# Performance work log

Measured on AMD Instinct MI355X. Metric: run time of the kernel, lower is better.

The kernel has to match this reference:

```python
import jax, jax.numpy as jnp
import numpy as np

N, E, D_IN, D_H, D_OUT, W = 100000, 1600000, 128, 128, 128, 3
HTC_W, TEMP = 0.01, 1.0  # curvature c = 1.0


def _project(x):
    n = jnp.maximum(jnp.linalg.norm(x, axis=-1, keepdims=True), 1e-12)
    return x * jnp.minimum((1.0 - 1e-5) / n, 1.0)


def _artanh(x):
    x = jnp.clip(x, -1.0 + 1e-6, 1.0 - 1e-6)
    return 0.5 * (jnp.log1p(x) - jnp.log1p(-x))


def _expmap0(v):
    n = jnp.maximum(jnp.linalg.norm(v, axis=-1, keepdims=True), 1e-12)
    return _project(jnp.tanh(n) * v / n)


def _logmap0(y):
    y = _project(y)
    n = jnp.maximum(jnp.linalg.norm(y, axis=-1, keepdims=True), 1e-12)
    return _artanh(n) * y / n


def setup_inputs() -> dict:
    key = jax.random.key(0)
    ks = jax.random.split(key, 24)
    x = jax.random.normal(ks[0], (N, D_IN), dtype=jnp.float32)
    edge_index = jax.random.randint(ks[1], (2, E), 0, N)
    t = jax.random.uniform(ks[2], (E,), dtype=jnp.float32)
    prev_hyp = _project(jax.random.normal(ks[3], (N, D_OUT), dtype=jnp.float32) * 0.05)
    lengths = jax.random.randint(ks[4], (N,), 0, W + 1)
    valid_mask = jnp.arange(W)[None, :] < lengths[:, None]  # front-filled deque
    hist_hyp = _project(jax.random.normal(ks[5], (N, W, D_OUT), dtype=jnp.float32) * 0.05)
    hist_hyp = hist_hyp * valid_mask[..., None].astype(jnp.float32)  # padded slots are zero

    def lin(k, dout, din):
        return jax.random.normal(k, (dout, din), dtype=jnp.float32) / np.sqrt(din)

    params = dict(
        w_time=jax.random.normal(ks[6], (D_IN,), dtype=jnp.float32),
        b_time=jnp.zeros((D_IN,), jnp.float32),
        W0_l=lin(ks[7], D_H, D_IN), b0_l=jnp.zeros((D_H,), jnp.float32), W0_r=lin(ks[8], D_H, D_IN),
        W1_l=lin(ks[9], D_OUT, D_H), b1_l=jnp.zeros((D_OUT,), jnp.float32), W1_r=lin(ks[10], D_OUT, D_H),
        W_ih=lin(ks[11], 3 * D_OUT, D_OUT), W_hh=lin(ks[12], 3 * D_OUT, D_OUT),
        b_ih=jnp.zeros((3 * D_OUT,), jnp.float32), b_hh=jnp.zeros((3 * D_OUT,), jnp.float32),
        Wq=lin(ks[13], D_OUT, D_OUT), Wk=lin(ks[14], D_OUT, D_OUT), Wv=lin(ks[15], D_OUT, D_OUT),
    )
    return dict(x=x, edge_index=edge_index, t=t, prev_hyp=prev_hyp,
                hist_hyp=hist_hyp, valid_mask=valid_mask, **params)


def reference(x, edge_index, t, prev_hyp, hist_hyp, valid_mask,
              w_time, b_time, W0_l, b0_l, W0_r, W1_l, b1_l, W1_r,
              W_ih, W_hh, b_ih, b_hh, Wq, Wk, Wv):
    n = x.shape[0]
    src, dst = edge_index[0], edge_index[1]
    ones_e = jnp.ones_like(t)
    # per-node mean event time over incident edges (src and dst both count)
    nt = jax.ops.segment_sum(t, src, n) + jax.ops.segment_sum(t, dst, n)
    cnt = jax.ops.segment_sum(ones_e, src, n) + jax.ops.segment_sum(ones_e, dst, n)
    node_time = nt / jnp.maximum(cnt, 1.0)
    x = x + jnp.cos(node_time[:, None] * w_time[None, :] + b_time[None, :])
    # SAGEConv (mean aggr over incoming edges): out = W_l @ mean_j x_j + b + W_r @ x_i
    deg = jnp.maximum(jax.ops.segment_sum(ones_e, dst, n), 1.0)[:, None]
    agg0 = jax.ops.segment_sum(x[src], dst, n) / deg
    h = jax.nn.relu(agg0 @ W0_l.T + b0_l + x @ W0_r.T)
    agg1 = jax.ops.segment_sum(h[src], dst, n) / deg
    h_now = agg1 @ W1_l.T + b1_l + h @ W1_r.T  # tangent-space current embedding

    prev_tan = _logmap0(prev_hyp)
    # ragged history attention (padded + masked)
    hist_tan = _logmap0(hist_hyp)                       # [N, W, D]
    q = h_now @ Wq.T                                    # [N, D]
    k = hist_tan @ Wk.T                                 # [N, W, D]
    v = hist_tan @ Wv.T
    score = jnp.einsum('nwd,nd->nw', k, q) / (np.sqrt(D_OUT) * max(TEMP, 1e-6))
    has_hist = valid_mask.any(axis=-1, keepdims=True)
    score = jnp.where(valid_mask, score, -jnp.inf)
    score = jnp.where(has_hist, score, 0.0)
    alpha = jax.nn.softmax(score, axis=-1)
    alpha = jnp.where(has_hist, alpha, 0.0)
    ctx = jnp.einsum('nw,nwd->nd', alpha, v)

    # GRUCell(input=h_now, hidden=prev_tan + ctx)
    hidden = prev_tan + ctx
    gi = h_now @ W_ih.T + b_ih
    gh = hidden @ W_hh.T + b_hh
    i_r, i_z, i_n = jnp.split(gi, 3, axis=-1)
    h_r, h_z, h_n = jnp.split(gh, 3, axis=-1)
    r = jax.nn.sigmoid(i_r + h_r)
    z = jax.nn.sigmoid(i_z + h_z)
    nn_ = jnp.tanh(i_n + r * h_n)
    h_tan = (1.0 - z) * nn_ + z * hidden
    h_hyp = _expmap0(h_tan)

    # hyperbolic temporal consistency aux loss (c = 1)
    x_sq = jnp.sum(h_hyp * h_hyp, axis=-1)
    y_sq = jnp.sum(prev_hyp * prev_hyp, axis=-1)
    diff_sq = jnp.sum((h_hyp - prev_hyp) ** 2, axis=-1)
    denom = jnp.maximum((1.0 - x_sq) * (1.0 - y_sq), 1e-8)
    zarg = jnp.maximum(1.0 + 2.0 * diff_sq / denom, 1.0 + 1e-6)
    dist = jnp.arccosh(zarg)
    valid_prev = (jnp.sum(jnp.abs(prev_hyp), axis=-1) > 0).astype(dist.dtype)
    aux = HTC_W * jnp.sum(dist * valid_prev) / jnp.maximum(jnp.sum(valid_prev), 1.0)
    aux = jnp.where(jnp.any(valid_prev > 0), aux, 0.0)
    return h_hyp, aux
```

## Files before the change

kernel.cpp:

```cpp
#include <hip/hip_runtime.h>
#include <math.h>


typedef _Float16 f16x8 __attribute__((ext_vector_type(8)));
typedef _Float16 f16x4 __attribute__((ext_vector_type(4)));
typedef _Float16 f16x2 __attribute__((ext_vector_type(2)));
typedef float f32x4 __attribute__((ext_vector_type(4)));

__device__ __forceinline__ float wsum(float v) {
#pragma unroll
  for (int off = 1; off < 64; off <<= 1) v += __shfl_xor(v, off, 64);
  return v;
}

__device__ __forceinline__ void fsplit(float x, _Float16& h, _Float16& l) {
  h = (_Float16)x;
  l = (_Float16)(x - (float)h);
}

__device__ __forceinline__ float logmap_scale(float nrm2) {
  float n0 = fmaxf(sqrtf(nrm2), 1e-12f);
  float sp = fminf((1.0f - 1e-5f) / n0, 1.0f);
  float np = fmaxf(n0 * sp, 1e-12f);
  float a  = fminf(np, 1.0f - 1e-6f);
  float at = 0.5f * (log1pf(a) - log1pf(-a));
  return sp * at / np;
}

__global__ void k_edge(const int* __restrict__ ei, const float* __restrict__ t,
                       unsigned long long* __restrict__ packed, int E) {
  int e = blockIdx.x * 256 + threadIdx.x;
  if (e >= E) return;
  int s = ei[e], d = ei[E + e];
  unsigned long long tf =
      (unsigned long long)__float2uint_rn(t[e] * 16777216.0f);
  unsigned long long encs = tf | (1ULL << 40);
  atomicAdd(&packed[s], encs);
  atomicAdd(&packed[d], encs | (1ULL << 52));
}

__global__ void k_scan1(const unsigned long long* __restrict__ packed,
                        int* __restrict__ rowptr, int* __restrict__ bsum, int N) {
  __shared__ int s[256];
  int t = threadIdx.x;
  int base = blockIdx.x * 1024 + t * 4;
  int v[4]; int loc = 0;
#pragma unroll
  for (int j = 0; j < 4; ++j) {
    int i = base + j;
    v[j] = (i < N) ? (int)(packed[i] >> 52) : 0;
    loc += v[j];
  }
  s[t] = loc; __syncthreads();
  for (int off = 1; off < 256; off <<= 1) {
    int x = (t >= off) ? s[t - off] : 0; __syncthreads();
    s[t] += x; __syncthreads();
  }
  int run = s[t] - loc;
#pragma unroll
  for (int j = 0; j < 4; ++j) { int i = base + j; if (i < N) rowptr[i] = run; run += v[j]; }
  if (t == 255) bsum[blockIdx.x] = s[255];
}

__global__ void k_scan2(const int* __restrict__ bsum, int* __restrict__ boff, int nb) {
  __shared__ int s[128];
  int t = threadIdx.x;
  int v = (t < nb) ? bsum[t] : 0;
  s[t] = v; __syncthreads();
  for (int off = 1; off < 128; off <<= 1) {
    int x = (t >= off) ? s[t - off] : 0; __syncthreads();
    s[t] += x; __syncthreads();
  }
  boff[t] = s[t] - v;
}

__global__ void k_scan3(int* __restrict__ rowptr, const int* __restrict__ boff, int N, int E) {
  int i = blockIdx.x * 256 + threadIdx.x;
  if (i < N) rowptr[i] += boff[i >> 10];
  if (i == 0) rowptr[N] = E;
}

__global__ void k_scatter(const int* __restrict__ ei, const int* __restrict__ rowptr,
                          int* __restrict__ cursor, int* __restrict__ eidx, int E) {
  int e = blockIdx.x * 256 + threadIdx.x;
  if (e >= E) return;
  int s = ei[e], d = ei[E + e];
  int p = rowptr[d] + atomicAdd(&cursor[d], 1);
  eidx[p] = s;
}

__global__ void k_time(const float* __restrict__ x,
                       const unsigned long long* __restrict__ packed,
                       const float* __restrict__ wt,
                       const float* __restrict__ bt,
                       _Float16* __restrict__ outH, _Float16* __restrict__ outL, int N) {
  int id = blockIdx.x * 256 + threadIdx.x;
  if (id >= N * 32) return;
  int n = id >> 5, q = id & 31;
  unsigned long long p = packed[n];
  float tsum = (float)(p & 0xFFFFFFFFFFULL) * 5.9604644775390625e-8f;
  int c = (int)((p >> 40) & 0xFFF);
  float tm = tsum / fmaxf((float)c, 1.0f);
  float4 xv = ((const float4*)x)[id];
  float4 wv = ((const float4*)wt)[q];
  float4 bv = ((const float4*)bt)[q];
  float o[4];
  o[0] = xv.x + cosf(tm * wv.x + bv.x);
  o[1] = xv.y + cosf(tm * wv.y + bv.y);
  o[2] = xv.z + cosf(tm * wv.z + bv.z);
  o[3] = xv.w + cosf(tm * wv.w + bv.w);
  f16x4 vh, vl;
#pragma unroll
  for (int j = 0; j < 4; ++j) { _Float16 h, l; fsplit(o[j], h, l); vh[j] = h; vl[j] = l; }
  *(f16x4*)&outH[(size_t)id * 4] = vh;
  *(f16x4*)&outL[(size_t)id * 4] = vl;
}

__global__ void k_agg(const _Float16* __restrict__ XH, const _Float16* __restrict__ XL,
                      const int* __restrict__ rowptr,
                      const int* __restrict__ eidx, _Float16* __restrict__ outH,
                      _Float16* __restrict__ outL, int N) {
  int wid = threadIdx.x >> 6, lane = threadIdx.x & 63;
  int n = blockIdx.x * 4 + wid;
  if (n >= N) return;
  int s0 = rowptr[n], s1 = rowptr[n + 1];
  size_t lo2 = (size_t)lane * 2;
  float ax0 = 0.f, ay0 = 0.f, ax1 = 0.f, ay1 = 0.f;
  float ax2 = 0.f, ay2 = 0.f, ax3 = 0.f, ay3 = 0.f;
  int e = s0;
  for (; e + 4 <= s1; e += 4) {
    int i0 = eidx[e], i1 = eidx[e + 1], i2 = eidx[e + 2], i3 = eidx[e + 3];
    f16x2 h0 = *(const f16x2*)&XH[(size_t)i0 * 128 + lo2];
    f16x2 l0 = *(const f16x2*)&XL[(size_t)i0 * 128 + lo2];
    f16x2 h1 = *(const f16x2*)&XH[(size_t)i1 * 128 + lo2];
    f16x2 l1 = *(const f16x2*)&XL[(size_t)i1 * 128 + lo2];
    f16x2 h2 = *(const f16x2*)&XH[(size_t)i2 * 128 + lo2];
    f16x2 l2 = *(const f16x2*)&XL[(size_t)i2 * 128 + lo2];
    f16x2 h3 = *(const f16x2*)&XH[(size_t)i3 * 128 + lo2];
    f16x2 l3 = *(const f16x2*)&XL[(size_t)i3 * 128 + lo2];
    ax0 += (float)h0[0] + (float)l0[0]; ay0 += (float)h0[1] + (float)l0[1];
    ax1 += (float)h1[0] + (float)l1[0]; ay1 += (float)h1[1] + (float)l1[1];
    ax2 += (float)h2[0] + (float)l2[0]; ay2 += (float)h2[1] + (float)l2[1];
    ax3 += (float)h3[0] + (float)l3[0]; ay3 += (float)h3[1] + (float)l3[1];
  }
  float ax = (ax0 + ax1) + (ax2 + ax3);
  float ay = (ay0 + ay1) + (ay2 + ay3);
  for (; e < s1; ++e) {
    int s = eidx[e];
    f16x2 vh = *(const f16x2*)&XH[(size_t)s * 128 + lo2];
    f16x2 vl = *(const f16x2*)&XL[(size_t)s * 128 + lo2];
    ax += (float)vh[0] + (float)vl[0];
    ay += (float)vh[1] + (float)vl[1];
  }
  float sc = 1.0f / fmaxf((float)(s1 - s0), 1.0f);
  _Float16 hx, lx, hy, ly;
  fsplit(ax * sc, hx, lx); fsplit(ay * sc, hy, ly);
  f16x2 vh = {hx, hy}, vl = {lx, ly};
  *(f16x2*)&outH[(size_t)n * 128 + lo2] = vh;
  *(f16x2*)&outL[(size_t)n * 128 + lo2] = vl;
}

__global__ void k_prep(const float* __restrict__ W0l, const float* __restrict__ W0r,
                       const float* __restrict__ W1l, const float* __restrict__ W1r,
                       const float* __restrict__ Wv,  const float* __restrict__ Wih,
                       const float* __restrict__ Whh, const float* __restrict__ bih,
                       const float* __restrict__ bhh,
                       _Float16* __restrict__ W0H, _Float16* __restrict__ W0L,
                       _Float16* __restrict__ W1H, _Float16* __restrict__ W1L,
                       _Float16* __restrict__ WvH, _Float16* __restrict__ WvL,
                       _Float16* __restrict__ WzH, _Float16* __restrict__ WzL,
                       float* __restrict__ bz) {
  int id = blockIdx.x * 256 + threadIdx.x;
  if (id < 32768) {
    int c = id >> 8, k = id & 255;
    float v0 = (k < 128) ? W0l[c * 128 + k] : W0r[c * 128 + (k - 128)];
    float v1 = (k < 128) ? W1l[c * 128 + k] : W1r[c * 128 + (k - 128)];
    fsplit(v0, W0H[id], W0L[id]);
    fsplit(v1, W1H[id], W1L[id]);
  }
  if (id < 16384) {
    fsplit(Wv[id], WvH[id], WvL[id]);
  }
  if (id < 131072) {
    int c = id >> 8, k = id & 255;
    float v;
    if (c < 256)      v = (k < 128) ? Wih[c * 128 + k] : Whh[c * 128 + (k - 128)];
    else if (c < 384) v = (k < 128) ? Wih[c * 128 + k] : 0.f;
    else              v = (k < 128) ? 0.f : Whh[(c - 128) * 128 + (k - 128)];
    fsplit(v, WzH[id], WzL[id]);
  }
  if (id < 512) {
    float v;
    if (id < 256)      v = bih[id] + bhh[id];
    else if (id < 384) v = bih[id];
    else               v = bhh[id - 128];
    bz[id] = v;
  }
}

__global__ void k_ct(const float* __restrict__ Wk, const float* __restrict__ Wq,
                     _Float16* __restrict__ CtH, _Float16* __restrict__ CtL) {
  int id = blockIdx.x * 256 + threadIdx.x;
  if (id >= 16384) return;
  int c = id >> 7, k = id & 127;
  float s = 0.f;
  for (int j = 0; j < 128; ++j) s += Wk[j * 128 + c] * Wq[j * 128 + k];
  fsplit(s, CtH[id], CtL[id]);
}

__global__ void k_lognorm(const float* __restrict__ Y, float* __restrict__ scale, int N) {
  int wid = threadIdx.x >> 6, lane = threadIdx.x & 63;
  int n = blockIdx.x * 4 + wid;
  if (n >= N) return;
  float2 y = ((const float2*)Y)[(size_t)n * 64 + lane];
  float nrm2 = wsum(y.x * y.x + y.y * y.y);
  if (lane == 0) scale[n] = logmap_scale(nrm2);
}

__global__ __launch_bounds__(256)
void k_mm(const _Float16* __restrict__ A1H, const _Float16* __restrict__ A1L,
          const _Float16* __restrict__ A2H, const _Float16* __restrict__ A2L,
          const _Float16* __restrict__ WH,  const _Float16* __restrict__ WL,
          const float* __restrict__ bias,   const float* __restrict__ addb,
          const float* __restrict__ scalev,
          float* __restrict__ outF, _Float16* __restrict__ outH,
          _Float16* __restrict__ outL,
          int Nrows, int Ktot, int Ctot, int relu) {
  __shared__ _Float16 sA[2][128][64];
  __shared__ _Float16 sW[2][128][64];
  const int tid = threadIdx.x;
  const int lane = tid & 63;
  const int wv = tid >> 6;
  const int wr = wv >> 1, wc = wv & 1;
  const int laneR = lane & 15, laneG = lane >> 4;
  const int n0 = blockIdx.x * 128;
  const int c0 = blockIdx.y * 128;

  f32x4 acc[4][4];
#pragma unroll
  for (int mi = 0; mi < 4; ++mi)
#pragma unroll
    for (int ni = 0; ni < 4; ++ni)
#pragma unroll
      for (int j = 0; j < 4; ++j) acc[mi][ni][j] = 0.f;

  const int nslab = Ktot >> 6;
  for (int s = 0; s < nslab; ++s) {
    int kglob = s << 6;
    const _Float16* aH = (kglob < 128) ? A1H : A2H;
    const _Float16* aL = (kglob < 128) ? A1L : A2L;
    int kc = kglob & 127;
    __syncthreads();
#pragma unroll
    for (int it = 0; it < 4; ++it) {
      int idx = tid + (it << 8);
      int r = idx >> 3, chunk = idx & 7;
      int cs = (chunk ^ (r & 7)) << 3;
      int kq = chunk << 3;
      int n = n0 + r;
      f16x8 vh, vl;
      if (n < Nrows) {
        vh = *(const f16x8*)&aH[(size_t)n * 128 + kc + kq];
        vl = *(const f16x8*)&aL[(size_t)n * 128 + kc + kq];
      } else {
#pragma unroll
        for (int j = 0; j < 8; ++j) { vh[j] = (_Float16)0; vl[j] = (_Float16)0; }
      }
      *(f16x8*)&sA[0][r][cs] = vh;
      *(f16x8*)&sA[1][r][cs] = vl;
      int c = c0 + r;
      f16x8 wh = *(const f16x8*)&WH[(size_t)c * Ktot + kglob + kq];
      f16x8 wl = *(const f16x8*)&WL[(size_t)c * Ktot + kglob + kq];
      *(f16x8*)&sW[0][r][cs] = wh;
      *(f16x8*)&sW[1][r][cs] = wl;
    }
    __syncthreads();
#pragma unroll
    for (int kk = 0; kk < 2; ++kk) {
      f16x8 ah[4], al[4], bh[4], bl[4];
      int kch = (kk << 2) + laneG;
#pragma unroll
      for (int m = 0; m < 4; ++m) {
        int row = wr * 64 + m * 16 + laneR;
        int ko = (kch ^ (row & 7)) << 3;
        ah[m] = *(const f16x8*)&sA[0][row][ko];
        al[m] = *(const f16x8*)&sA[1][row][ko];
      }
#pragma unroll
      for (int n = 0; n < 4; ++n) {
        int row = wc * 64 + n * 16 + laneR;
        int ko = (kch ^ (row & 7)) << 3;
        bh[n] = *(const f16x8*)&sW[0][row][ko];
        bl[n] = *(const f16x8*)&sW[1][row][ko];
      }
#pragma unroll
      for (int m = 0; m < 4; ++m)
#pragma unroll
        for (int n = 0; n < 4; ++n) {
          acc[m][n] = __builtin_amdgcn_mfma_f32_16x16x32_f16(ah[m], bh[n], acc[m][n], 0, 0, 0);
          acc[m][n] = __builtin_amdgcn_mfma_f32_16x16x32_f16(al[m], bh[n], acc[m][n], 0, 0, 0);
          acc[m][n] = __builtin_amdgcn_mfma_f32_16x16x32_f16(ah[m], bl[n], acc[m][n], 0, 0, 0);
        }
    }
  }
#pragma unroll
  for (int m = 0; m < 4; ++m) {
#pragma unroll
    for (int n = 0; n < 4; ++n) {
      int rbase = n0 + wr * 64 + m * 16 + laneG * 4;
      int c = c0 + wc * 64 + n * 16 + laneR;
      float bval = bias ? bias[c] : 0.f;
#pragma unroll
      for (int j = 0; j < 4; ++j) {
        int r = rbase + j;
        if (r >= Nrows) continue;
        float v = acc[m][n][j] + bval;
        if (addb) {
          float ab = addb[(size_t)r * Ctot + c];
          v += scalev ? ab * scalev[r] : ab;
        }
        if (relu) v = fmaxf(v, 0.f);
        if (outF) outF[(size_t)r * Ctot + c] = v;
        if (outH) {
          _Float16 h, l; fsplit(v, h, l);
          outH[(size_t)r * Ctot + c] = h;
          outL[(size_t)r * Ctot + c] = l;
        }
      }
    }
  }
}

__global__ __launch_bounds__(256, 2)
void k_uattn(const _Float16* __restrict__ AH, const _Float16* __restrict__ AL,
             const _Float16* __restrict__ WH, const _Float16* __restrict__ WL,
             const float* __restrict__ hist,
             _Float16* __restrict__ outH, _Float16* __restrict__ outL, int N) {
  __shared__ __align__(16) char smem[65536];
  _Float16 (*sA)[128][64] = (_Float16(*)[128][64])smem;
  _Float16 (*sW)[128][64] = (_Float16(*)[128][64])(smem + 32768);
  float (*uS)[128] = (float(*)[128])smem;
  const int tid = threadIdx.x;
  const int lane = tid & 63;
  const int wv = tid >> 6;
  const int wr = wv >> 1, wc = wv & 1;
  const int laneR = lane & 15, laneG = lane >> 4;
  const int n0 = blockIdx.x * 128;

  f32x4 acc[4][4];
#pragma unroll
  for (int mi = 0; mi < 4; ++mi)
#pragma unroll
    for (int ni = 0; ni < 4; ++ni)
#pragma unroll
      for (int j = 0; j < 4; ++j) acc[mi][ni][j] = 0.f;

  for (int s = 0; s < 2; ++s) {
    int kglob = s << 6;
    __syncthreads();
#pragma unroll
    for (int it = 0; it < 4; ++it) {
      int idx = tid + (it << 8);
      int r = idx >> 3, chunk = idx & 7;
      int cs = (chunk ^ (r & 7)) << 3;
      int kq = chunk << 3;
      int n = n0 + r;
      f16x8 vh, vl;
      if (n < N) {
        vh = *(const f16x8*)&AH[(size_t)n * 128 + kglob + kq];
        vl = *(const f16x8*)&AL[(size_t)n * 128 + kglob + kq];
      } else {
#pragma unroll
        for (int j = 0; j < 8; ++j) { vh[j] = (_Float16)0; vl[j] = (_Float16)0; }
      }
      *(f16x8*)&sA[0][r][cs] = vh;
      *(f16x8*)&sA[1][r][cs] = vl;
      f16x8 wh = *(const f16x8*)&WH[(size_t)r * 128 + kglob + kq];
      f16x8 wl = *(const f16x8*)&WL[(size_t)r * 128 + kglob + kq];
      *(f16x8*)&sW[0][r][cs] = wh;
      *(f16x8*)&sW[1][r][cs] = wl;
    }
    __syncthreads();
#pragma unroll
    for (int kk = 0; kk < 2; ++kk) {
      f16x8 ah[4], al[4], bh[4], bl[4];
      int kch = (kk << 2) + laneG;
#pragma unroll
      for (int m = 0; m < 4; ++m) {
        int row = wr * 64 + m * 16 + laneR;
        int ko = (kch ^ (row & 7)) << 3;
        ah[m] = *(const f16x8*)&sA[0][row][ko];
        al[m] = *(const f16x8*)&sA[1][row][ko];
      }
#pragma unroll
      for (int n = 0; n < 4; ++n) {
        int row = wc * 64 + n * 16 + laneR;
        int ko = (kch ^ (row & 7)) << 3;
        bh[n] = *(const f16x8*)&sW[0][row][ko];
        bl[n] = *(const f16x8*)&sW[1][row][ko];
      }
#pragma unroll
      for (int m = 0; m < 4; ++m)
#pragma unroll
        for (int n = 0; n < 4; ++n) {
          acc[m][n] = __builtin_amdgcn_mfma_f32_16x16x32_f16(ah[m], bh[n], acc[m][n], 0, 0, 0);
          acc[m][n] = __builtin_amdgcn_mfma_f32_16x16x32_f16(al[m], bh[n], acc[m][n], 0, 0, 0);
          acc[m][n] = __builtin_amdgcn_mfma_f32_16x16x32_f16(ah[m], bl[n], acc[m][n], 0, 0, 0);
        }
    }
  }
  __syncthreads();
#pragma unroll
  for (int m = 0; m < 4; ++m)
#pragma unroll
    for (int n = 0; n < 4; ++n) {
      int rl = wr * 64 + m * 16 + laneG * 4;
      int c = wc * 64 + n * 16 + laneR;
#pragma unroll
      for (int j = 0; j < 4; ++j) uS[rl + j][c] = acc[m][n][j];
    }
  __syncthreads();

  for (int i = 0; i < 32; ++i) {
    int rl = wv * 32 + i;
    int n = n0 + rl;
    if (n >= N) break;
    float2 u = *(const float2*)&uS[rl][lane * 2];
    float htx[3], hty[3], sc[3];
    bool val[3];
#pragma unroll
    for (int w = 0; w < 3; ++w) {
      float2 h = ((const float2*)hist)[((size_t)n * 3 + w) * 64 + lane];
      float nrm2 = wsum(h.x * h.x + h.y * h.y);
      val[w] = nrm2 > 0.f;
      float s = logmap_scale(nrm2);
      htx[w] = h.x * s; hty[w] = h.y * s;
      float d = wsum(htx[w] * u.x + hty[w] * u.y);
      sc[w] = d * 0.0883883476483184f;
    }
    float cx = 0.f, cy = 0.f;
    if (val[0] || val[1] || val[2]) {
      float m = -INFINITY;
#pragma unroll
      for (int w = 0; w < 3; ++w) if (val[w]) m = fmaxf(m, sc[w]);
      float a[3]; float ssum = 0.f;
#pragma unroll
      for (int w = 0; w < 3; ++w) { a[w] = val[w] ? expf(sc[w] - m) : 0.f; ssum += a[w]; }
      float inv = 1.f / ssum;
#pragma unroll
      for (int w = 0; w < 3; ++w) { cx += htx[w] * (a[w] * inv); cy += hty[w] * (a[w] * inv); }
    }
    _Float16 hx, lx, hy, ly;
    fsplit(cx, hx, lx); fsplit(cy, hy, ly);
    f16x2 vh = {hx, hy}, vl = {lx, ly};
    *(f16x2*)&outH[(size_t)n * 128 + lane * 2] = vh;
    *(f16x2*)&outL[(size_t)n * 128 + lane * 2] = vl;
  }
}

__global__ __launch_bounds__(256, 2)
void k_gru(const _Float16* __restrict__ P0H, const _Float16* __restrict__ P0L,
           const _Float16* __restrict__ P2H, const _Float16* __restrict__ P2L,
           const _Float16* __restrict__ WzH, const _Float16* __restrict__ WzL,
           const float* __restrict__ bz, const float* __restrict__ prev,
           float* __restrict__ out, float* __restrict__ pd,
           float* __restrict__ pv, int N) {
  __shared__ _Float16 sA[2][64][64];
  __shared__ _Float16 sW[2][128][64];
  __shared__ float rn1[64][2];
  __shared__ float rn3[64][2][3];
  __shared__ float distrow[64], validrow[64];
  const int tid = threadIdx.x;
  const int lane = tid & 63;
  const int wv = tid >> 6;
  const int wr = wv >> 1, wc = wv & 1;
  const int laneR = lane & 15, laneG = lane >> 4;
  const int n0 = blockIdx.x * 64;

  f32x4 acc[4][2][4];
#pragma unroll
  for (int q = 0; q < 4; ++q)
#pragma unroll
    for (int m = 0; m < 2; ++m)
#pragma unroll
      for (int n = 0; n < 4; ++n)
#pragma unroll
        for (int j = 0; j < 4; ++j) acc[q][m][n][j] = 0.f;

#define STAGE_W(Q)                                                          \
  {                                                                         \
    _Pragma("unroll")                                                       \
    for (int it = 0; it < 4; ++it) {                                        \
      int idx = tid + (it << 8);                                            \
      int r = idx >> 3, chunk = idx & 7;                                    \
      int cs = (chunk ^ (r & 7)) << 3;                                      \
      int kq = chunk << 3;                                                  \
      size_t wrow = (size_t)((Q)*128 + r);                                  \
      *(f16x8*)&sW[0][r][cs] = *(const f16x8*)&WzH[wrow * 256 + kglob + kq];\
      *(f16x8*)&sW[1][r][cs] = *(const f16x8*)&WzL[wrow * 256 + kglob + kq];\
    }                                                                       \
  }

#define COMPUTE_Q(Q)                                                        \
  {                                                                         \
    _Pragma("unroll")                                                       \
    for (int kk = 0; kk < 2; ++kk) {                                        \
      int kch = (kk << 2) + laneG;                                          \
      f16x8 ah[2], al[2], bh[4], bl[4];                                     \
      _Pragma("unroll")                                                     \
      for (int m = 0; m < 2; ++m) {                                         \
        int row = wr * 32 + m * 16 + laneR;                                 \
        int ko = (kch ^ (row & 7)) << 3;                                    \
        ah[m] = *(const f16x8*)&sA[0][row][ko];                             \
        al[m] = *(const f16x8*)&sA[1][row][ko];                             \
      }                                                                     \
      _Pragma("unroll")                                                     \
      for (int n = 0; n < 4; ++n) {                                         \
        int row = wc * 64 + n * 16 + laneR;                                 \
        int ko = (kch ^ (row & 7)) << 3;                                    \
        bh[n] = *(const f16x8*)&sW[0][row][ko];                             \
        bl[n] = *(const f16x8*)&sW[1][row][ko];                             \
      }                                                                     \
      _Pragma("unroll")                                                     \
      for (int m = 0; m < 2; ++m)                                           \
        _Pragma("unroll")                                                   \
        for (int n = 0; n < 4; ++n) {                                       \
          acc[Q][m][n] = __builtin_amdgcn_mfma_f32_16x16x32_f16(ah[m], bh[n], acc[Q][m][n], 0, 0, 0); \
          acc[Q][m][n] = __builtin_amdgcn_mfma_f32_16x16x32_f16(al[m], bh[n], acc[Q][m][n], 0, 0, 0); \
          acc[Q][m][n] = __builtin_amdgcn_mfma_f32_16x16x32_f16(ah[m], bl[n], acc[Q][m][n], 0, 0, 0); \
        }                                                                   \
    }                                                                       \
  }

#pragma unroll
  for (int s = 0; s < 4; ++s) {
    int kglob = s << 6;
    const _Float16* aH = (s < 2) ? P0H : P2H;
    const _Float16* aL = (s < 2) ? P0L : P2L;
    int kc = kglob & 127;
    __syncthreads();
#pragma unroll
    for (int it = 0; it < 2; ++it) {
      int idx = tid + (it << 8);
      int r = idx >> 3, chunk = idx & 7;
      int cs = (chunk ^ (r & 7)) << 3;
      int kq = chunk << 3;
      int n = n0 + r;
      f16x8 vh, vl;
      if (n < N) {
        vh = *(const f16x8*)&aH[(size_t)n * 128 + kc + kq];
        vl = *(const f16x8*)&aL[(size_t)n * 128 + kc + kq];
      } else {
#pragma unroll
        for (int j = 0; j < 8; ++j) { vh[j] = (_Float16)0; vl[j] = (_Float16)0; }
      }
      *(f16x8*)&sA[0][r][cs] = vh;
      *(f16x8*)&sA[1][r][cs] = vl;
    }
    STAGE_W(0);
    __syncthreads();
    COMPUTE_Q(0);
    __syncthreads();
    STAGE_W(1);
    __syncthreads();
    COMPUTE_Q(1);
    __syncthreads();
    if (s < 2) {
      STAGE_W(2);
      __syncthreads();
      COMPUTE_Q(2);
    } else {
      STAGE_W(3);
      __syncthreads();
      COMPUTE_Q(3);
    }
  }
#undef STAGE_W
#undef COMPUTE_Q

  float bz0[4], bz1[4], bz2[4], bz3[4];
#pragma unroll
  for (int n = 0; n < 4; ++n) {
    int d = wc * 64 + n * 16 + laneR;
    bz0[n] = bz[d]; bz1[n] = bz[128 + d]; bz2[n] = bz[256 + d]; bz3[n] = bz[384 + d];
  }
  float tv[2][4][4];
#pragma unroll
  for (int m = 0; m < 2; ++m)
#pragma unroll
    for (int n = 0; n < 4; ++n)
#pragma unroll
      for (int j = 0; j < 4; ++j) {
        int row = n0 + wr * 32 + m * 16 + laneG * 4 + j;
        int d = wc * 64 + n * 16 + laneR;
        float hid = 0.f;
        if (row < N) {
          size_t o = (size_t)row * 128 + d;
          hid = (float)P2H[o] + (float)P2L[o];
        }
        float gr = acc[0][m][n][j] + bz0[n];
        float gz = acc[1][m][n][j] + bz1[n];
        float gi = acc[2][m][n][j] + bz2[n];
        float gh = acc[3][m][n][j] + bz3[n];
        float rr = 1.f / (1.f + expf(-gr));
        float zz = 1.f / (1.f + expf(-gz));
        float nn = tanhf(gi + rr * gh);
        tv[m][n][j] = (1.f - zz) * nn + zz * hid;
      }
#pragma unroll
  for (int m = 0; m < 2; ++m)
#pragma unroll
    for (int j = 0; j < 4; ++j) {
      float p = 0.f;
#pragma unroll
      for (int n = 0; n < 4; ++n) p += tv[m][n][j] * tv[m][n][j];
#pragma unroll
      for (int off = 1; off < 16; off <<= 1) p += __shfl_xor(p, off, 64);
      if (laneR == 0) rn1[wr * 32 + m * 16 + laneG * 4 + j][wc] = p;
    }
  __syncthreads();
  float hv[2][4][4];
#pragma unroll
  for (int m = 0; m < 2; ++m)
#pragma unroll
    for (int j = 0; j < 4; ++j) {
      int rl = wr * 32 + m * 16 + laneG * 4 + j;
      int row = n0 + rl;
      float nv2 = rn1[rl][0] + rn1[rl][1];
      float nv = fmaxf(sqrtf(nv2), 1e-12f);
      float tn = tanhf(nv);
      float s1 = tn / nv;
      float nw = fmaxf(tn, 1e-12f);
      float sp = fminf((1.f - 1e-5f) / nw, 1.f);
      float scl = s1 * sp;
#pragma unroll
      for (int n = 0; n < 4; ++n) {
        float h = tv[m][n][j] * scl;
        hv[m][n][j] = h;
        int d = wc * 64 + n * 16 + laneR;
        if (row < N) out[(size_t)row * 128 + d] = h;
      }
    }
#pragma unroll
  for (int m = 0; m < 2; ++m)
#pragma unroll
    for (int j = 0; j < 4; ++j) {
      int rl = wr * 32 + m * 16 + laneG * 4 + j;
      int row = n0 + rl;
      float ys = 0.f, ds = 0.f, pa = 0.f;
#pragma unroll
      for (int n = 0; n < 4; ++n) {
        int d = wc * 64 + n * 16 + laneR;
        float p = (row < N) ? prev[(size_t)row * 128 + d] : 0.f;
        float h = hv[m][n][j];
        ys += p * p; ds += (h - p) * (h - p); pa += fabsf(p);
      }
#pragma unroll
      for (int off = 1; off < 16; off <<= 1) {
        ys += __shfl_xor(ys, off, 64);
        ds += __shfl_xor(ds, off, 64);
        pa += __shfl_xor(pa, off, 64);
      }
      if (laneR == 0) { rn3[rl][wc][0] = ys; rn3[rl][wc][1] = ds; rn3[rl][wc][2] = pa; }
    }
  __syncthreads();
  if (wc == 0 && laneR == 0) {
#pragma unroll
    for (int m = 0; m < 2; ++m)
#pragma unroll
      for (int j = 0; j < 4; ++j) {
        int rl = wr * 32 + m * 16 + laneG * 4 + j;
        int row = n0 + rl;
        float nv2 = rn1[rl][0] + rn1[rl][1];
        float nv = fmaxf(sqrtf(nv2), 1e-12f);
        float tn = tanhf(nv);
        float s1 = tn / nv;
        float nw = fmaxf(tn, 1e-12f);
        float sp = fminf((1.f - 1e-5f) / nw, 1.f);
        float scl = s1 * sp;
        float x_sq = scl * scl * nv2;
        float y_sq = rn3[rl][0][0] + rn3[rl][1][0];
        float d_sq = rn3[rl][0][1] + rn3[rl][1][1];
        float pab  = rn3[rl][0][2] + rn3[rl][1][2];
        float denom = fmaxf((1.f - x_sq) * (1.f - y_sq), 1e-8f);
        float zarg = fmaxf(1.f + 2.f * d_sq / denom, 1.f + 1e-6f);
        float dist = acoshf(zarg);
        float valid = (pab > 0.f && row < N) ? 1.f : 0.f;
        distrow[rl] = dist * valid;
        validrow[rl] = valid;
      }
  }
  __syncthreads();
  if (tid < 64) {
    float dv = distrow[tid], vvv = validrow[tid];
    dv = wsum(dv); vvv = wsum(vvv);
    if (tid == 0) { pd[blockIdx.x] = dv; pv[blockIdx.x] = vvv; }
  }
}

__global__ void k_reduce(const float* __restrict__ pd, const float* __restrict__ pv,
                         float* __restrict__ aux_out, int nparts) {
  __shared__ float sd[256], sv[256];
  float a = 0.f, b = 0.f;
  for (int i = threadIdx.x; i < nparts; i += 256) { a += pd[i]; b += pv[i]; }
  sd[threadIdx.x] = a; sv[threadIdx.x] = b; __syncthreads();
  for (int off = 128; off > 0; off >>= 1) {
    if (threadIdx.x < off) { sd[threadIdx.x] += sd[threadIdx.x + off]; sv[threadIdx.x] += sv[threadIdx.x + off]; }
    __syncthreads();
  }
  if (threadIdx.x == 0) {
    float aux = (sv[0] > 0.f) ? 0.01f * sd[0] / fmaxf(sv[0], 1.f) : 0.f;
    aux_out[0] = aux;
  }
}

extern "C" void kernel_launch(void* const* d_in, const int* in_sizes, int n_in,
                              void* d_out, int out_size, void* d_ws, size_t ws_size,
                              hipStream_t stream) {
  const float* x      = (const float*)d_in[0];
  const int*   ei     = (const int*)  d_in[1];
  const float* t      = (const float*)d_in[2];
  const float* prev   = (const float*)d_in[3];
  const float* hist   = (const float*)d_in[4];
  const float* w_time = (const float*)d_in[6];
  const float* b_time = (const float*)d_in[7];
  const float* W0l    = (const float*)d_in[8];
  const float* b0l    = (const float*)d_in[9];
  const float* W0r    = (const float*)d_in[10];
  const float* W1l    = (const float*)d_in[11];
  const float* b1l    = (const float*)d_in[12];
  const float* W1r    = (const float*)d_in[13];
  const float* Wih    = (const float*)d_in[14];
  const float* Whh    = (const float*)d_in[15];
  const float* bih    = (const float*)d_in[16];
  const float* bhh    = (const float*)d_in[17];
  const float* Wq     = (const float*)d_in[18];
  const float* Wk     = (const float*)d_in[19];
  const float* Wv     = (const float*)d_in[20];

  const int N = in_sizes[0] / 128;
  const int E = in_sizes[1] / 2;
  const int NB4 = (N + 3) / 4;
  const int NB1 = (N + 1023) / 1024;
  const int NBG = (N + 63) / 64;

  char* wbase = (char*)d_ws;
  size_t off = 0;
  auto alloc = [&](size_t bytes) -> void* {
    off = (off + 255) & ~(size_t)255;
    void* p = wbase + off; off += bytes; return p;
  };
  unsigned long long* packed = (unsigned long long*)alloc((size_t)N * 8);
  int*   cursor = (int*)  alloc((size_t)N * 4);
  size_t zero_bytes = off;
  int*   rowptr = (int*)  alloc((size_t)(N + 1) * 4);
  int*   bsum   = (int*)  alloc(512);
  int*   boff   = (int*)  alloc(512);
  int*   eidx   = (int*)  alloc((size_t)E * 4);
  _Float16* W0H = (_Float16*)alloc(32768 * 2);
  _Float16* W0L = (_Float16*)alloc(32768 * 2);
  _Float16* W1H = (_Float16*)alloc(32768 * 2);
  _Float16* W1L = (_Float16*)alloc(32768 * 2);
  _Float16* CtH = (_Float16*)alloc(16384 * 2);
  _Float16* CtL = (_Float16*)alloc(16384 * 2);
  _Float16* WvH = (_Float16*)alloc(16384 * 2);
  _Float16* WvL = (_Float16*)alloc(16384 * 2);
  _Float16* WzH = (_Float16*)alloc(131072 * 2);
  _Float16* WzL = (_Float16*)alloc(131072 * 2);
  float* bz     = (float*)alloc(512 * 4);
  float* scale  = (float*)alloc((size_t)N * 4);
  _Float16* P0H = (_Float16*)alloc((size_t)N * 128 * 2);
  _Float16* P0L = (_Float16*)alloc((size_t)N * 128 * 2);
  _Float16* P1H = (_Float16*)alloc((size_t)N * 128 * 2);
  _Float16* P1L = (_Float16*)alloc((size_t)N * 128 * 2);
  _Float16* P2H = (_Float16*)alloc((size_t)N * 128 * 2);
  _Float16* P2L = (_Float16*)alloc((size_t)N * 128 * 2);
  float* pd = (float*)alloc((size_t)NBG * 4);
  float* pv = (float*)alloc((size_t)NBG * 4);
  (void)ws_size; (void)n_in; (void)out_size;

  float* out_h   = (float*)d_out;
  float* out_aux = out_h + (size_t)N * 128;

  hipMemsetAsync(d_ws, 0, zero_bytes, stream);

  k_prep<<<512, 256, 0, stream>>>(W0l, W0r, W1l, W1r, Wv, Wih, Whh, bih, bhh,
                                  W0H, W0L, W1H, W1L, WvH, WvL, WzH, WzL, bz);
  k_ct<<<64, 256, 0, stream>>>(Wk, Wq, CtH, CtL);
  k_lognorm<<<NB4, 256, 0, stream>>>(prev, scale, N);

  int ebl = (E + 255) / 256;
  k_edge<<<ebl, 256, 0, stream>>>(ei, t, packed, E);
  k_scan1<<<NB1, 256, 0, stream>>>(packed, rowptr, bsum, N);
  k_scan2<<<1, 128, 0, stream>>>(bsum, boff, NB1);
  k_scan3<<<(N + 255) / 256, 256, 0, stream>>>(rowptr, boff, N, E);
  k_scatter<<<ebl, 256, 0, stream>>>(ei, rowptr, cursor, eidx, E);

  k_time<<<(N * 32 + 255) / 256, 256, 0, stream>>>(x, packed, w_time, b_time,
                                                   P0H, P0L, N);
  k_agg<<<NB4, 256, 0, stream>>>(P0H, P0L, rowptr, eidx, P1H, P1L, N);
  dim3 gb((N + 127) / 128, 1);
  k_mm<<<gb, 256, 0, stream>>>(P1H, P1L, P0H, P0L, W0H, W0L, b0l, nullptr, nullptr,
                               nullptr, P2H, P2L, N, 256, 128, 1);
  k_agg<<<NB4, 256, 0, stream>>>(P2H, P2L, rowptr, eidx, P1H, P1L, N);
  k_mm<<<gb, 256, 0, stream>>>(P1H, P1L, P2H, P2L, W1H, W1L, b1l, nullptr, nullptr,
                               nullptr, P0H, P0L, N, 256, 128, 0);
  k_uattn<<<gb, 256, 0, stream>>>(P0H, P0L, CtH, CtL, hist, P1H, P1L, N);
  k_mm<<<gb, 256, 0, stream>>>(P1H, P1L, nullptr, nullptr, WvH, WvL, nullptr, prev,
                               scale, nullptr, P2H, P2L, N, 128, 128, 0);
  k_gru<<<NBG, 256, 0, stream>>>(P0H, P0L, P2H, P2L, WzH, WzL, bz, prev,
                                 out_h, pd, pv, N);
  k_reduce<<<1, 256, 0, stream>>>(pd, pv, out_aux, NBG);
}
```

Before: 1.215 ms.

## Interleave hi/lo f16 splits per row and fuse layer-1 GEMM with query projection

The separate hi and lo f16 buffers become one interleaved row of 256 halves per node. The gather in k_agg then fetches hi and lo together in one 8-byte load per lane, touching one contiguous 512-byte row instead of two separate rows. The layer-1 GEMM is fused with the Ct projection in a new k_mmu kernel that writes the split output and an fp32 U buffer. The attention softmax becomes its own per-node kernel, k_attn. This trades an extra fp32 N×128 buffer write and read, plus another launch, for fewer scattered gather transactions and less work packed into one kernel.

```diff
diff --git a/kernel.cpp b/kernel.cpp
--- a/kernel.cpp
+++ b/kernel.cpp
@@ -93,7 +93,7 @@
                        const unsigned long long* __restrict__ packed,
                        const float* __restrict__ wt,
                        const float* __restrict__ bt,
-                       _Float16* __restrict__ outH, _Float16* __restrict__ outL, int N) {
+                       _Float16* __restrict__ out, int N) {
   int id = blockIdx.x * 256 + threadIdx.x;
   if (id >= N * 32) return;
   int n = id >> 5, q = id & 31;
@@ -112,52 +112,56 @@
   f16x4 vh, vl;
 #pragma unroll
   for (int j = 0; j < 4; ++j) { _Float16 h, l; fsplit(o[j], h, l); vh[j] = h; vl[j] = l; }
-  *(f16x4*)&outH[(size_t)id * 4] = vh;
-  *(f16x4*)&outL[(size_t)id * 4] = vl;
-}
-
-__global__ void k_agg(const _Float16* __restrict__ XH, const _Float16* __restrict__ XL,
-                      const int* __restrict__ rowptr,
-                      const int* __restrict__ eidx, _Float16* __restrict__ outH,
-                      _Float16* __restrict__ outL, int N) {
+  *(f16x4*)&out[(size_t)n * 256 + q * 4] = vh;
+  *(f16x4*)&out[(size_t)n * 256 + 128 + q * 4] = vl;
+}
+
+__global__ void k_agg(const _Float16* __restrict__ X, const int* __restrict__ rowptr,
+                      const int* __restrict__ eidx, _Float16* __restrict__ out, int N) {
   int wid = threadIdx.x >> 6, lane = threadIdx.x & 63;
   int n = blockIdx.x * 4 + wid;
   if (n >= N) return;
   int s0 = rowptr[n], s1 = rowptr[n + 1];
-  size_t lo2 = (size_t)lane * 2;
-  float ax0 = 0.f, ay0 = 0.f, ax1 = 0.f, ay1 = 0.f;
-  float ax2 = 0.f, ay2 = 0.f, ax3 = 0.f, ay3 = 0.f;
+  size_t lo4 = (size_t)lane * 4;
+  float a0[4] = {0, 0, 0, 0}, a1[4] = {0, 0, 0, 0};
+  float a2[4] = {0, 0, 0, 0}, a3[4] = {0, 0, 0, 0};
   int e = s0;
   for (; e + 4 <= s1; e += 4) {
     int i0 = eidx[e], i1 = eidx[e + 1], i2 = eidx[e + 2], i3 = eidx[e + 3];
-    f16x2 h0 = *(const f16x2*)&XH[(size_t)i0 * 128 + lo2];
-    f16x2 l0 = *(const f16x2*)&XL[(size_t)i0 * 128 + lo2];
-    f16x2 h1 = *(const f16x2*)&XH[(size_t)i1 * 128 + lo2];
-    f16x2 l1 = *(const f16x2*)&XL[(size_t)i1 * 128 + lo2];
-    f16x2 h2 = *(const f16x2*)&XH[(size_t)i2 * 128 + lo2];
-    f16x2 l2 = *(const f16x2*)&XL[(size_t)i2 * 128 + lo2];
-    f16x2 h3 = *(const f16x2*)&XH[(size_t)i3 * 128 + lo2];
-    f16x2 l3 = *(const f16x2*)&XL[(size_t)i3 * 128 + lo2];
-    ax0 += (float)h0[0] + (float)l0[0]; ay0 += (float)h0[1] + (float)l0[1];
-    ax1 += (float)h1[0] + (float)l1[0]; ay1 += (float)h1[1] + (float)l1[1];
-    ax2 += (float)h2[0] + (float)l2[0]; ay2 += (float)h2[1] + (float)l2[1];
-    ax3 += (float)h3[0] + (float)l3[0]; ay3 += (float)h3[1] + (float)l3[1];
-  }
-  float ax = (ax0 + ax1) + (ax2 + ax3);
-  float ay = (ay0 + ay1) + (ay2 + ay3);
+    f16x4 v0 = *(const f16x4*)&X[(size_t)i0 * 256 + lo4];
+    f16x4 v1 = *(const f16x4*)&X[(size_t)i1 * 256 + lo4];
+    f16x4 v2 = *(const f16x4*)&X[(size_t)i2 * 256 + lo4];
+    f16x4 v3 = *(const f16x4*)&X[(size_t)i3 * 256 + lo4];
+#pragma unroll
+    for (int j = 0; j < 4; ++j) {
+      a0[j] += (float)v0[j]; a1[j] += (float)v1[j];
+      a2[j] += (float)v2[j]; a3[j] += (float)v3[j];
+    }
+  }
+  float a[4];
+#pragma unroll
+  for (int j = 0; j < 4; ++j) a[j] = (a0[j] + a1[j]) + (a2[j] + a3[j]);
   for (; e < s1; ++e) {
     int s = eidx[e];
-    f16x2 vh = *(const f16x2*)&XH[(size_t)s * 128 + lo2];
-    f16x2 vl = *(const f16x2*)&XL[(size_t)s * 128 + lo2];
-    ax += (float)vh[0] + (float)vl[0];
-    ay += (float)vh[1] + (float)vl[1];
-  }
-  float sc = 1.0f / fmaxf((float)(s1 - s0), 1.0f);
-  _Float16 hx, lx, hy, ly;
-  fsplit(ax * sc, hx, lx); fsplit(ay * sc, hy, ly);
-  f16x2 vh = {hx, hy}, vl = {lx, ly};
-  *(f16x2*)&outH[(size_t)n * 128 + lo2] = vh;
-  *(f16x2*)&outL[(size_t)n * 128 + lo2] = vl;
+    f16x4 v = *(const f16x4*)&X[(size_t)s * 256 + lo4];
+#pragma unroll
+    for (int j = 0; j < 4; ++j) a[j] += (float)v[j];
+  }
+  float lov[4];
+#pragma unroll
+  for (int j = 0; j < 4; ++j) lov[j] = __shfl(a[j], lane + 32, 64);
+  if (lane < 32) {
+    float sc = 1.0f / fmaxf((float)(s1 - s0), 1.0f);
+    f16x4 vh, vl;
+#pragma unroll
+    for (int j = 0; j < 4; ++j) {
+      float v = (a[j] + lov[j]) * sc;
+      _Float16 h, l; fsplit(v, h, l);
+      vh[j] = h; vl[j] = l;
+    }
+    *(f16x4*)&out[(size_t)n * 256 + lane * 4] = vh;
+    *(f16x4*)&out[(size_t)n * 256 + 128 + lane * 4] = vl;
+  }
 }
 
 __global__ void k_prep(const float* __restrict__ W0l, const float* __restrict__ W0r,
@@ -218,13 +222,11 @@
 }
 
 __global__ __launch_bounds__(256)
-void k_mm(const _Float16* __restrict__ A1H, const _Float16* __restrict__ A1L,
-          const _Float16* __restrict__ A2H, const _Float16* __restrict__ A2L,
+void k_mm(const _Float16* __restrict__ A1, const _Float16* __restrict__ A2,
           const _Float16* __restrict__ WH,  const _Float16* __restrict__ WL,
           const float* __restrict__ bias,   const float* __restrict__ addb,
           const float* __restrict__ scalev,
-          float* __restrict__ outF, _Float16* __restrict__ outH,
-          _Float16* __restrict__ outL,
+          float* __restrict__ outF, _Float16* __restrict__ outS,
           int Nrows, int Ktot, int Ctot, int relu) {
   __shared__ _Float16 sA[2][128][64];
   __shared__ _Float16 sW[2][128][64];
@@ -247,8 +249,7 @@
   const int nslab = Ktot >> 6;
   for (int s = 0; s < nslab; ++s) {
     int kglob = s << 6;
-    const _Float16* aH = (kglob < 128) ? A1H : A2H;
-    const _Float16* aL = (kglob < 128) ? A1L : A2L;
+    const _Float16* Ax = (kglob < 128) ? A1 : A2;
     int kc = kglob & 127;
     __syncthreads();
 #pragma unroll
@@ -260,8 +261,8 @@
       int n = n0 + r;
       f16x8 vh, vl;
       if (n < Nrows) {
-        vh = *(const f16x8*)&aH[(size_t)n * 128 + kc + kq];
-        vl = *(const f16x8*)&aL[(size_t)n * 128 + kc + kq];
+        vh = *(const f16x8*)&Ax[(size_t)n * 256 + kc + kq];
+        vl = *(const f16x8*)&Ax[(size_t)n * 256 + 128 + kc + kq];
       } else {
 #pragma unroll
         for (int j = 0; j < 8; ++j) { vh[j] = (_Float16)0; vl[j] = (_Float16)0; }
@@ -321,25 +322,24 @@
         }
         if (relu) v = fmaxf(v, 0.f);
         if (outF) outF[(size_t)r * Ctot + c] = v;
-        if (outH) {
+        if (outS) {
           _Float16 h, l; fsplit(v, h, l);
-          outH[(size_t)r * Ctot + c] = h;
-          outL[(size_t)r * Ctot + c] = l;
+          outS[(size_t)r * 256 + c] = h;
+          outS[(size_t)r * 256 + 128 + c] = l;
         }
       }
     }
   }
 }
 
-__global__ __launch_bounds__(256, 2)
-void k_uattn(const _Float16* __restrict__ AH, const _Float16* __restrict__ AL,
-             const _Float16* __restrict__ WH, const _Float16* __restrict__ WL,
-             const float* __restrict__ hist,
-             _Float16* __restrict__ outH, _Float16* __restrict__ outL, int N) {
-  __shared__ __align__(16) char smem[65536];
-  _Float16 (*sA)[128][64] = (_Float16(*)[128][64])smem;
-  _Float16 (*sW)[128][64] = (_Float16(*)[128][64])(smem + 32768);
-  float (*uS)[128] = (float(*)[128])smem;
+__global__ __launch_bounds__(256)
+void k_mmu(const _Float16* __restrict__ A1, const _Float16* __restrict__ A2,
+           const _Float16* __restrict__ WH, const _Float16* __restrict__ WL,
+           const _Float16* __restrict__ CtH, const _Float16* __restrict__ CtL,
+           const float* __restrict__ bias,
+           _Float16* __restrict__ outS, float* __restrict__ outU, int Nrows) {
+  __shared__ _Float16 sA[2][128][64];
+  __shared__ _Float16 sW[2][128][64];
   const int tid = threadIdx.x;
   const int lane = tid & 63;
   const int wv = tid >> 6;
@@ -355,8 +355,10 @@
 #pragma unroll
       for (int j = 0; j < 4; ++j) acc[mi][ni][j] = 0.f;
 
-  for (int s = 0; s < 2; ++s) {
+  for (int s = 0; s < 4; ++s) {
     int kglob = s << 6;
+    const _Float16* Ax = (kglob < 128) ? A1 : A2;
+    int kc = kglob & 127;
     __syncthreads();
 #pragma unroll
     for (int it = 0; it < 4; ++it) {
@@ -366,17 +368,17 @@
       int kq = chunk << 3;
       int n = n0 + r;
       f16x8 vh, vl;
-      if (n < N) {
-        vh = *(const f16x8*)&AH[(size_t)n * 128 + kglob + kq];
-        vl = *(const f16x8*)&AL[(size_t)n * 128 + kglob + kq];
+      if (n < Nrows) {
+        vh = *(const f16x8*)&Ax[(size_t)n * 256 + kc + kq];
+        vl = *(const f16x8*)&Ax[(size_t)n * 256 + 128 + kc + kq];
       } else {
 #pragma unroll
         for (int j = 0; j < 8; ++j) { vh[j] = (_Float16)0; vl[j] = (_Float16)0; }
       }
       *(f16x8*)&sA[0][r][cs] = vh;
       *(f16x8*)&sA[1][r][cs] = vl;
-      f16x8 wh = *(const f16x8*)&WH[(size_t)r * 128 + kglob + kq];
-      f16x8 wl = *(const f16x8*)&WL[(size_t)r * 128 + kglob + kq];
+      f16x8 wh = *(const f16x8*)&WH[(size_t)r * 256 + kglob + kq];
+      f16x8 wl = *(const f16x8*)&WL[(size_t)r * 256 + kglob + kq];
       *(f16x8*)&sW[0][r][cs] = wh;
       *(f16x8*)&sW[1][r][cs] = wl;
     }
@@ -409,58 +411,134 @@
         }
     }
   }
-  __syncthreads();
-#pragma unroll
-  for (int m = 0; m < 4; ++m)
+
+  f32x4 accU[4][4];
+#pragma unroll
+  for (int mi = 0; mi < 4; ++mi)
+#pragma unroll
+    for (int ni = 0; ni < 4; ++ni)
+#pragma unroll
+      for (int j = 0; j < 4; ++j) accU[mi][ni][j] = 0.f;
+
+  for (int us = 0; us < 2; ++us) {
+    __syncthreads();
+    if (wc == us) {
+#pragma unroll
+      for (int m = 0; m < 4; ++m)
+#pragma unroll
+        for (int n = 0; n < 4; ++n) {
+          int kp = n * 16 + laneR;
+          float bval = bias[us * 64 + n * 16 + laneR];
+#pragma unroll
+          for (int j = 0; j < 4; ++j) {
+            int row = wr * 64 + m * 16 + laneG * 4 + j;
+            float v = acc[m][n][j] + bval;
+            _Float16 h, l; fsplit(v, h, l);
+            int cs = ((kp >> 3) ^ (row & 7)) * 8 + (kp & 7);
+            sA[0][row][cs] = h;
+            sA[1][row][cs] = l;
+          }
+        }
+    }
+#pragma unroll
+    for (int it = 0; it < 4; ++it) {
+      int idx = tid + (it << 8);
+      int r = idx >> 3, chunk = idx & 7;
+      int cs = (chunk ^ (r & 7)) << 3;
+      int kq = chunk << 3;
+      *(f16x8*)&sW[0][r][cs] = *(const f16x8*)&CtH[(size_t)r * 128 + us * 64 + kq];
+      *(f16x8*)&sW[1][r][cs] = *(const f16x8*)&CtL[(size_t)r * 128 + us * 64 + kq];
+    }
+    __syncthreads();
+#pragma unroll
+    for (int kk = 0; kk < 2; ++kk) {
+      f16x8 ah[4], al[4], bh[4], bl[4];
+      int kch = (kk << 2) + laneG;
+#pragma unroll
+      for (int m = 0; m < 4; ++m) {
+        int row = wr * 64 + m * 16 + laneR;
+        int ko = (kch ^ (row & 7)) << 3;
+        ah[m] = *(const f16x8*)&sA[0][row][ko];
+        al[m] = *(const f16x8*)&sA[1][row][ko];
+      }
+#pragma unroll
+      for (int n = 0; n < 4; ++n) {
+        int row = wc * 64 + n * 16 + laneR;
+        int ko = (kch ^ (row & 7)) << 3;
+        bh[n] = *(const f16x8*)&sW[0][row][ko];
+        bl[n] = *(const f16x8*)&sW[1][row][ko];
+      }
+#pragma unroll
+      for (int m = 0; m < 4; ++m)
+#pragma unroll
+        for (int n = 0; n < 4; ++n) {
+          accU[m][n] = __builtin_amdgcn_mfma_f32_16x16x32_f16(ah[m], bh[n], accU[m][n], 0, 0, 0);
+          accU[m][n] = __builtin_amdgcn_mfma_f32_16x16x32_f16(al[m], bh[n], accU[m][n], 0, 0, 0);
+          accU[m][n] = __builtin_amdgcn_mfma_f32_16x16x32_f16(ah[m], bl[n], accU[m][n], 0, 0, 0);
+        }
+    }
+  }
+
+#pragma unroll
+  for (int m = 0; m < 4; ++m) {
 #pragma unroll
     for (int n = 0; n < 4; ++n) {
-      int rl = wr * 64 + m * 16 + laneG * 4;
+      int rbase = n0 + wr * 64 + m * 16 + laneG * 4;
       int c = wc * 64 + n * 16 + laneR;
-#pragma unroll
-      for (int j = 0; j < 4; ++j) uS[rl + j][c] = acc[m][n][j];
-    }
-  __syncthreads();
-
-  for (int i = 0; i < 32; ++i) {
-    int rl = wv * 32 + i;
-    int n = n0 + rl;
-    if (n >= N) break;
-    float2 u = *(const float2*)&uS[rl][lane * 2];
-    float htx[3], hty[3], sc[3];
-    bool val[3];
-#pragma unroll
-    for (int w = 0; w < 3; ++w) {
-      float2 h = ((const float2*)hist)[((size_t)n * 3 + w) * 64 + lane];
-      float nrm2 = wsum(h.x * h.x + h.y * h.y);
-      val[w] = nrm2 > 0.f;
-      float s = logmap_scale(nrm2);
-      htx[w] = h.x * s; hty[w] = h.y * s;
-      float d = wsum(htx[w] * u.x + hty[w] * u.y);
-      sc[w] = d * 0.0883883476483184f;
-    }
-    float cx = 0.f, cy = 0.f;
-    if (val[0] || val[1] || val[2]) {
-      float m = -INFINITY;
-#pragma unroll
-      for (int w = 0; w < 3; ++w) if (val[w]) m = fmaxf(m, sc[w]);
-      float a[3]; float ssum = 0.f;
-#pragma unroll
-      for (int w = 0; w < 3; ++w) { a[w] = val[w] ? expf(sc[w] - m) : 0.f; ssum += a[w]; }
-      float inv = 1.f / ssum;
-#pragma unroll
-      for (int w = 0; w < 3; ++w) { cx += htx[w] * (a[w] * inv); cy += hty[w] * (a[w] * inv); }
-    }
-    _Float16 hx, lx, hy, ly;
-    fsplit(cx, hx, lx); fsplit(cy, hy, ly);
-    f16x2 vh = {hx, hy}, vl = {lx, ly};
-    *(f16x2*)&outH[(size_t)n * 128 + lane * 2] = vh;
-    *(f16x2*)&outL[(size_t)n * 128 + lane * 2] = vl;
-  }
+      float bval = bias[c];
+#pragma unroll
+      for (int j = 0; j < 4; ++j) {
+        int r = rbase + j;
+        if (r >= Nrows) continue;
+        float v = acc[m][n][j] + bval;
+        _Float16 h, l; fsplit(v, h, l);
+        outS[(size_t)r * 256 + c] = h;
+        outS[(size_t)r * 256 + 128 + c] = l;
+        outU[(size_t)r * 128 + c] = accU[m][n][j];
+      }
+    }
+  }
+}
+
+__global__ void k_attn(const float* __restrict__ U, const float* __restrict__ hist,
+                       _Float16* __restrict__ out, int N) {
+  int wid = threadIdx.x >> 6, lane = threadIdx.x & 63;
+  int n = blockIdx.x * 4 + wid;
+  if (n >= N) return;
+  float2 u = ((const float2*)U)[(size_t)n * 64 + lane];
+  float htx[3], hty[3], sc[3];
+  bool val[3];
+#pragma unroll
+  for (int w = 0; w < 3; ++w) {
+    float2 h = ((const float2*)hist)[((size_t)n * 3 + w) * 64 + lane];
+    float nrm2 = wsum(h.x * h.x + h.y * h.y);
+    val[w] = nrm2 > 0.f;
+    float s = logmap_scale(nrm2);
+    htx[w] = h.x * s; hty[w] = h.y * s;
+    float d = wsum(htx[w] * u.x + hty[w] * u.y);
+    sc[w] = d * 0.0883883476483184f;
+  }
+  float cx = 0.f, cy = 0.f;
+  if (val[0] || val[1] || val[2]) {
+    float m = -INFINITY;
+#pragma unroll
+    for (int w = 0; w < 3; ++w) if (val[w]) m = fmaxf(m, sc[w]);
+    float a[3]; float ssum = 0.f;
+#pragma unroll
+    for (int w = 0; w < 3; ++w) { a[w] = val[w] ? expf(sc[w] - m) : 0.f; ssum += a[w]; }
+    float inv = 1.f / ssum;
+#pragma unroll
+    for (int w = 0; w < 3; ++w) { cx += htx[w] * (a[w] * inv); cy += hty[w] * (a[w] * inv); }
+  }
+  _Float16 hx, lx, hy, ly;
+  fsplit(cx, hx, lx); fsplit(cy, hy, ly);
+  f16x2 vh = {hx, hy}, vl = {lx, ly};
+  *(f16x2*)&out[(size_t)n * 256 + lane * 2] = vh;
+  *(f16x2*)&out[(size_t)n * 256 + 128 + lane * 2] = vl;
 }
 
 __global__ __launch_bounds__(256, 2)
-void k_gru(const _Float16* __restrict__ P0H, const _Float16* __restrict__ P0L,
-           const _Float16* __restrict__ P2H, const _Float16* __restrict__ P2L,
+void k_gru(const _Float16* __restrict__ P0c, const _Float16* __restrict__ P2c,
            const _Float16* __restrict__ WzH, const _Float16* __restrict__ WzL,
            const float* __restrict__ bz, const float* __restrict__ prev,
            float* __restrict__ out, float* __restrict__ pd,
@@ -535,8 +613,7 @@
 #pragma unroll
   for (int s = 0; s < 4; ++s) {
     int kglob = s << 6;
-    const _Float16* aH = (s < 2) ? P0H : P2H;
-    const _Float16* aL = (s < 2) ? P0L : P2L;
+    const _Float16* Ax = (s < 2) ? P0c : P2c;
     int kc = kglob & 127;
     __syncthreads();
 #pragma unroll
@@ -548,8 +625,8 @@
       int n = n0 + r;
       f16x8 vh, vl;
       if (n < N) {
-        vh = *(const f16x8*)&aH[(size_t)n * 128 + kc + kq];
-        vl = *(const f16x8*)&aL[(size_t)n * 128 + kc + kq];
+        vh = *(const f16x8*)&Ax[(size_t)n * 256 + kc + kq];
+        vl = *(const f16x8*)&Ax[(size_t)n * 256 + 128 + kc + kq];
       } else {
 #pragma unroll
         for (int j = 0; j < 8; ++j) { vh[j] = (_Float16)0; vl[j] = (_Float16)0; }
@@ -595,8 +672,8 @@
         int d = wc * 64 + n * 16 + laneR;
         float hid = 0.f;
         if (row < N) {
-          size_t o = (size_t)row * 128 + d;
-          hid = (float)P2H[o] + (float)P2L[o];
+          size_t o = (size_t)row * 256 + d;
+          hid = (float)P2c[o] + (float)P2c[o + 128];
         }
         float gr = acc[0][m][n][j] + bz0[n];
         float gz = acc[1][m][n][j] + bz1[n];
@@ -769,12 +846,10 @@
   _Float16* WzL = (_Float16*)alloc(131072 * 2);
   float* bz     = (float*)alloc(512 * 4);
   float* scale  = (float*)alloc((size_t)N * 4);
-  _Float16* P0H = (_Float16*)alloc((size_t)N * 128 * 2);
-  _Float16* P0L = (_Float16*)alloc((size_t)N * 128 * 2);
-  _Float16* P1H = (_Float16*)alloc((size_t)N * 128 * 2);
-  _Float16* P1L = (_Float16*)alloc((size_t)N * 128 * 2);
-  _Float16* P2H = (_Float16*)alloc((size_t)N * 128 * 2);
-  _Float16* P2L = (_Float16*)alloc((size_t)N * 128 * 2);
+  float* F0     = (float*)alloc((size_t)N * 128 * 4);
+  _Float16* P0c = (_Float16*)alloc((size_t)N * 256 * 2);
+  _Float16* P1c = (_Float16*)alloc((size_t)N * 256 * 2);
+  _Float16* P2c = (_Float16*)alloc((size_t)N * 256 * 2);
   float* pd = (float*)alloc((size_t)NBG * 4);
   float* pv = (float*)alloc((size_t)NBG * 4);
   (void)ws_size; (void)n_in; (void)out_size;
@@ -797,18 +872,17 @@
   k_scatter<<<ebl, 256, 0, stream>>>(ei, rowptr, cursor, eidx, E);
 
   k_time<<<(N * 32 + 255) / 256, 256, 0, stream>>>(x, packed, w_time, b_time,
-                                                   P0H, P0L, N);
-  k_agg<<<NB4, 256, 0, stream>>>(P0H, P0L, rowptr, eidx, P1H, P1L, N);
+                                                   P0c, N);
+  k_agg<<<NB4, 256, 0, stream>>>(P0c, rowptr, eidx, P1c, N);
   dim3 gb((N + 127) / 128, 1);
-  k_mm<<<gb, 256, 0, stream>>>(P1H, P1L, P0H, P0L, W0H, W0L, b0l, nullptr, nullptr,
-                               nullptr, P2H, P2L, N, 256, 128, 1);
-  k_agg<<<NB4, 256, 0, stream>>>(P2H, P2L, rowptr, eidx, P1H, P1L, N);
-  k_mm<<<gb, 256, 0, stream>>>(P1H, P1L, P2H, P2L, W1H, W1L, b1l, nullptr, nullptr,
-                               nullptr, P0H, P0L, N, 256, 128, 0);
-  k_uattn<<<gb, 256, 0, stream>>>(P0H, P0L, CtH, CtL, hist, P1H, P1L, N);
-  k_mm<<<gb, 256, 0, stream>>>(P1H, P1L, nullptr, nullptr, WvH, WvL, nullptr, prev,
-                               scale, nullptr, P2H, P2L, N, 128, 128, 0);
-  k_gru<<<NBG, 256, 0, stream>>>(P0H, P0L, P2H, P2L, WzH, WzL, bz, prev,
+  k_mm<<<gb, 256, 0, stream>>>(P1c, P0c, W0H, W0L, b0l, nullptr, nullptr,
+                               nullptr, P2c, N, 256, 128, 1);
+  k_agg<<<NB4, 256, 0, stream>>>(P2c, rowptr, eidx, P1c, N);
+  k_mmu<<<gb, 256, 0, stream>>>(P1c, P2c, W1H, W1L, CtH, CtL, b1l, P0c, F0, N);
+  k_attn<<<NB4, 256, 0, stream>>>(F0, hist, P1c, N);
+  k_mm<<<gb, 256, 0, stream>>>(P1c, nullptr, WvH, WvL, nullptr, prev, scale,
+                               nullptr, P2c, N, 128, 128, 0);
+  k_gru<<<NBG, 256, 0, stream>>>(P0c, P2c, WzH, WzL, bz, prev,
                                  out_h, pd, pv, N);
   k_reduce<<<1, 256, 0, stream>>>(pd, pv, out_aux, NBG);
 }
```

After: 1.122 ms, median of 2. -7.7%, faster.
